# Kernel tuning notes

Hardware: AMD Instinct MI355X
Metric: run time of the kernel (lower is better)

The kernel has to match this reference:

```python
import jax, jax.numpy as jnp
import numpy as np

H, C, PQ, PV = 12, 16, 4, 8
CN = 384
INF, EPS = 1e5, 1e-7


def setup_inputs() -> dict:
    key = jax.random.key(0)
    ks = jax.random.split(key, 12)
    B, N = 2, 768
    s = jax.random.normal(ks[0], (B, N, CN), jnp.float32)
    m = jax.random.normal(ks[1], (B, N, 3, 3), jnp.float32)
    rot, _ = jnp.linalg.qr(m)  # proper orthonormal frames
    trans = jax.random.normal(ks[2], (B, N, 3), jnp.float32)
    pair_mask = jnp.ones((B, N, N), jnp.float32)
    sc = 0.02
    hc = H * C
    w_q = jax.random.normal(ks[3], (hc, CN), jnp.float32) * sc
    b_q = jnp.zeros((hc,), jnp.float32)
    w_kv = jax.random.normal(ks[4], (2 * hc, CN), jnp.float32) * sc
    b_kv = jnp.zeros((2 * hc,), jnp.float32)
    w_qp = jax.random.normal(ks[5], (H * PQ * 3, CN), jnp.float32) * sc
    b_qp = jnp.zeros((H * PQ * 3,), jnp.float32)
    w_kvp = jax.random.normal(ks[6], (H * (PQ + PV) * 3, CN), jnp.float32) * sc
    b_kvp = jnp.zeros((H * (PQ + PV) * 3,), jnp.float32)
    head_weights = jnp.full((H,), float(np.log(np.e - 1.0)), jnp.float32)  # softplus -> 1
    cod = H * (C + PV * 4)
    w_out = jax.random.normal(ks[7], (CN, cod), jnp.float32) * sc
    b_out = jnp.zeros((CN,), jnp.float32)
    return dict(s=s, rot=rot, trans=trans, pair_mask=pair_mask,
                w_q=w_q, b_q=b_q, w_kv=w_kv, b_kv=b_kv,
                w_qp=w_qp, b_qp=b_qp, w_kvp=w_kvp, b_kvp=b_kvp,
                head_weights=head_weights, w_out=w_out, b_out=b_out)


def reference(s, rot, trans, pair_mask, w_q, b_q, w_kv, b_kv, w_qp, b_qp,
              w_kvp, b_kvp, head_weights, w_out, b_out):
    B, N, _ = s.shape
    q = (s @ w_q.T + b_q).reshape(B, N, H, C)
    kv = (s @ w_kv.T + b_kv).reshape(B, N, H, 2 * C)
    k, v = kv[..., :C], kv[..., C:]

    def point_proj(wf, bf, P):
        p = s @ wf.T + bf                                   # [B,N,H*P*3]
        p = jnp.stack(jnp.split(p, 3, axis=-1), axis=-1)     # [B,N,H*P,3]
        p = jnp.einsum('bnxy,bnpy->bnpx', rot, p) + trans[:, :, None, :]
        return p.reshape(B, N, H, P, 3)

    q_pts = point_proj(w_qp, b_qp, PQ)
    kv_pts = point_proj(w_kvp, b_kvp, PQ + PV)
    k_pts, v_pts = kv_pts[..., :PQ, :], kv_pts[..., PQ:, :]

    a = jnp.einsum('bihc,bjhc->bhij', q, k) * (1.0 / (3 * C)) ** 0.5
    # [B,N,N,H,PQ] squared point distances (the big intermediate)
    d2 = jnp.sum((q_pts[:, :, None] - k_pts[:, None]) ** 2, axis=-1)
    hw = jax.nn.softplus(head_weights) * (1.0 / (3 * (PQ * 9.0 / 2))) ** 0.5
    pt_att = -0.5 * jnp.sum(d2 * hw[:, None], axis=-1)      # [B,N,N,H]
    a = a + jnp.transpose(pt_att, (0, 3, 1, 2)) + (INF * (pair_mask - 1.0))[:, None]
    a = jax.nn.softmax(a, axis=-1)                          # [B,H,N,N]

    o = jnp.einsum('bhij,bjhc->bihc', a, v).reshape(B, N, H * C)
    o_pt = jnp.einsum('bhij,bjhpc->bihpc', a, v_pts)        # [B,N,H,PV,3]
    o_pt = jnp.einsum('bnyx,bnhpy->bnhpx', rot, o_pt - trans[:, :, None, None, :])
    o_pt_norm = jnp.sqrt(jnp.sum(o_pt ** 2, axis=-1) + EPS).reshape(B, N, H * PV)
    o_pt = o_pt.reshape(B, N, H * PV, 3)
    cat = jnp.concatenate([o, o_pt[..., 0], o_pt[..., 1], o_pt[..., 2], o_pt_norm], axis=-1)
    return cat @ w_out.T + b_out
```

## Files before the change

### kernel.cpp

```cpp
#include <hip/hip_runtime.h>
#include <hip/hip_bf16.h>
#include <math.h>

typedef __attribute__((ext_vector_type(4)))  short short4v;
typedef __attribute__((ext_vector_type(8)))  short short8;
typedef __attribute__((ext_vector_type(16))) float f32x16;

#define B_   2
#define N_   768
#define CN_  384
#define H_   12
#define INF_ 100000.0f
#define EPS_ 1e-7f

#define OFF_PROJP 0
#define OFF_O     884736
#define OFF_OP    1032192
#define OFF_CAT   1253376
#define OFF_QF    1769472
#define OFF_KF    2064384
#define OFF_VT    2359296
#define OFF_SB    2949120
#define OFF_WB    3244032
#define OFF_WOB   3465216
#define OFF_MB    3575808

__device__ inline float b2f(unsigned short u) {
    union { unsigned int i; float f; } x; x.i = ((unsigned int)u) << 16; return x.f;
}
__device__ inline unsigned short f2b(float f) {
    __hip_bfloat16 h = __float2bfloat16(f);
    return *reinterpret_cast<unsigned short*>(&h);
}

__global__ __launch_bounds__(256) void prep_kernel(
    const float* __restrict__ s,
    const float* __restrict__ w_q,  const float* __restrict__ w_kv,
    const float* __restrict__ w_qp, const float* __restrict__ w_kvp,
    const float* __restrict__ w_out,
    unsigned short* __restrict__ SB, unsigned short* __restrict__ WB,
    unsigned short* __restrict__ WOBT)
{
    const long i4 = ((long)blockIdx.x * 256 + threadIdx.x) * 4;
    const float* src; unsigned short* dst; long off;
    if (i4 < 589824) {
        src = s + i4; dst = SB; off = i4;
    } else if (i4 < 1032192) {
        long e = i4 - 589824;
        int row = (int)(e / 384), c = (int)(e - (long)row * 384);
        const float* wsrc;
        if (row < 192)      wsrc = w_q   + (long)row * 384;
        else if (row < 576) wsrc = w_kv  + (long)(row - 192) * 384;
        else if (row < 720) wsrc = w_qp  + (long)(row - 576) * 384;
        else                wsrc = w_kvp + (long)(row - 720) * 384;
        src = wsrc + c; dst = WB; off = e;
    } else {
        long e = i4 - 1032192;
        int row = (int)(e / 576), c = (int)(e - (long)row * 576);
        src = w_out + e; dst = WOBT;
        off = (((long)(row >> 5) * 72 + (c >> 3)) * 32 + (row & 31)) * 8 + (c & 7);
    }
    float4 v = *(const float4*)src;
    short4v o;
    o[0] = (short)f2b(v.x); o[1] = (short)f2b(v.y);
    o[2] = (short)f2b(v.z); o[3] = (short)f2b(v.w);
    *(short4v*)(dst + off) = o;
}

__global__ __launch_bounds__(64) void proj_mb_kernel(
    const unsigned short* __restrict__ SB, const unsigned short* __restrict__ WB,
    const float* __restrict__ b_q,  const float* __restrict__ b_kv,
    const float* __restrict__ b_qp, const float* __restrict__ b_kvp,
    const float* __restrict__ mask,
    float* __restrict__ PROJP, unsigned short* __restrict__ Qf,
    unsigned short* __restrict__ Kf, unsigned short* __restrict__ Vt,
    unsigned short* __restrict__ MB)
{
    if (blockIdx.x >= 1728) {
        const int tile = blockIdx.x - 1728;
        const int jt = tile % 24;
        const int it = (tile / 24) % 24;
        const int b  = tile / 576;
        const int tt = threadIdx.x;
        const int i0 = it * 32, j0 = jt * 32;
        const float* mrow = mask + ((long)b * N_ + i0 + (tt & 31)) * N_
                          + j0 + (tt >> 5) * 4;
        union { unsigned short u[16]; short8 v[2]; } o;
        #pragma unroll
        for (int g = 0; g < 4; ++g) {
            float4 mv = *(const float4*)(mrow + 8 * g);
            o.u[g*4+0] = f2b(INF_ * (mv.x - 1.f));
            o.u[g*4+1] = f2b(INF_ * (mv.y - 1.f));
            o.u[g*4+2] = f2b(INF_ * (mv.z - 1.f));
            o.u[g*4+3] = f2b(INF_ * (mv.w - 1.f));
        }
        unsigned short* outp = MB + (long)tile * 1024 + tt * 16;
        *(short8*)(outp)     = o.v[0];
        *(short8*)(outp + 8) = o.v[1];
        return;
    }
    const int tile = blockIdx.x;
    const int tn = tile % 36, tm = tile / 36;
    const int r0 = tm * 32, c0 = tn * 32;
    const int l  = threadIdx.x;
    const int li = l & 31, hf = l >> 5;

    const unsigned short* ap = SB + (long)(r0 + li) * CN_ + hf * 8;
    const int col = c0 + li;
    const unsigned short* wb = WB + (long)col * CN_ + hf * 8;
    const float bias = (col < 192) ? b_q[col] : (col < 576) ? b_kv[col - 192]
                     : (col < 720) ? b_qp[col - 576] : b_kvp[col - 720];

    f32x16 acc = {};
    for (int k = 0; k < CN_; k += 32) {
        short8 a0 = *(const short8*)(ap + k);
        short8 a1 = *(const short8*)(ap + k + 16);
        short8 b0 = *(const short8*)(wb + k);
        short8 b1 = *(const short8*)(wb + k + 16);
        acc = __builtin_amdgcn_mfma_f32_32x32x16_bf16(a0, b0, acc, 0, 0, 0);
        acc = __builtin_amdgcn_mfma_f32_32x32x16_bf16(a1, b1, acc, 0, 0, 0);
    }
    const int row_b = r0 / N_;
    if (tn < 6) {
        const int hq = col >> 4, c = col & 15;
        const long qb = (long)(row_b * H_ + hq) * N_;
        #pragma unroll
        for (int r = 0; r < 16; ++r) {
            int row = r0 + (r & 3) + 8 * (r >> 2) + 4 * hf;
            int n = row - row_b * N_;
            Qf[(qb + n) * 32 + c] = f2b((acc[r] + bias) * 0.144337567297406f);
        }
    } else if (tn < 18) {
        const int hkv = tn - 6;
        const long kb = (long)(row_b * H_ + hkv) * N_;
        const long vb = (long)(row_b * H_ + hkv) * 24;
        #pragma unroll
        for (int r = 0; r < 16; ++r) {
            int row = r0 + (r & 3) + 8 * (r >> 2) + 4 * hf;
            int n = row - row_b * N_;
            unsigned short v = f2b(acc[r] + bias);
            if (li < 16) Kf[(kb + n) * 32 + li] = v;
            else Vt[((vb + (n >> 5)) * 64 + (li - 16)) * 32 + (n & 31)] = v;
        }
    } else {
        const int pc = col - 576;
        #pragma unroll
        for (int r = 0; r < 16; ++r) {
            int row = r0 + (r & 3) + 8 * (r >> 2) + 4 * hf;
            PROJP[(long)row * 576 + pc] = acc[r] + bias;
        }
    }
}

__global__ __launch_bounds__(128) void pack3_kernel(
    const float* __restrict__ PROJP,
    const float* __restrict__ rot, const float* __restrict__ trans,
    const float* __restrict__ head_weights,
    unsigned short* __restrict__ Qf, unsigned short* __restrict__ Kf,
    unsigned short* __restrict__ Vt)
{
    __shared__ float pp[576];
    __shared__ float rt[12];
    __shared__ float hws[12];
    __shared__ float kp2[48];
    const int bn = blockIdx.x;
    const int t  = threadIdx.x;
    const float4* src = (const float4*)(PROJP + (long)bn * 576);
    for (int d = t; d < 144; d += 128) ((float4*)pp)[d] = src[d];
    if (t < 9) rt[t]     = rot[bn * 9 + t];
    if (t < 3) rt[9 + t] = trans[bn * 3 + t];
    if (t < 12) {
        float v  = head_weights[t];
        float sp = (v > 20.f) ? v : log1pf(expf(v));
        hws[t] = sp * 0.13608276348795434f;
    }
    __syncthreads();
    const int b = bn / N_, n = bn % N_;
    for (int e = t; e < 192; e += 128) {
        if (e < 48) {
            int h = e >> 2, p = e & 3;
            float r0 = pp[     h * 4 + p];
            float r1 = pp[48 + h * 4 + p];
            float r2 = pp[96 + h * 4 + p];
            long base = ((long)(b * H_ + h) * N_ + n) * 32;
            #pragma unroll
            for (int x = 0; x < 3; ++x) {
                float o = rt[x*3]*r0 + rt[x*3+1]*r1 + rt[x*3+2]*r2 + rt[9+x];
                Qf[base + 16 + p * 3 + x] = f2b(o * hws[h]);
            }
        } else {
            int idx = e - 48;
            int h = idx / 12, pi = idx - h * 12;
            float r0 = pp[144 +       h * 12 + pi];
            float r1 = pp[144 + 144 + h * 12 + pi];
            float r2 = pp[144 + 288 + h * 12 + pi];
            float o0 = rt[0]*r0 + rt[1]*r1 + rt[2]*r2 + rt[9];
            float o1 = rt[3]*r0 + rt[4]*r1 + rt[5]*r2 + rt[10];
            float o2 = rt[6]*r0 + rt[7]*r1 + rt[8]*r2 + rt[11];
            if (pi < 4) {
                long base = ((long)(b * H_ + h) * N_ + n) * 32;
                Kf[base + 16 + pi * 3 + 0] = f2b(o0);
                Kf[base + 16 + pi * 3 + 1] = f2b(o1);
                Kf[base + 16 + pi * 3 + 2] = f2b(o2);
                kp2[h * 4 + pi] = o0*o0 + o1*o1 + o2*o2;
            } else {
                int dd = 16 + (pi - 4) * 3;
                long vb = ((long)(b * H_ + h) * 24 + (n >> 5)) * 64;
                Vt[(vb + dd + 0) * 32 + (n & 31)] = f2b(o0);
                Vt[(vb + dd + 1) * 32 + (n & 31)] = f2b(o1);
                Vt[(vb + dd + 2) * 32 + (n & 31)] = f2b(o2);
            }
        }
    }
    __syncthreads();
    if (t < 12) {
        float s2 = kp2[t*4] + kp2[t*4+1] + kp2[t*4+2] + kp2[t*4+3];
        float kc = -0.5f * hws[t] * s2;
        long base = ((long)(b * H_ + t) * N_ + n) * 32;
        unsigned short hi = f2b(kc);
        Kf[base + 28] = hi;
        Kf[base + 29] = f2b(kc - b2f(hi));
        Kf[base + 30] = 0; Kf[base + 31] = 0;
        unsigned short one = f2b(1.f);
        Qf[base + 28] = one; Qf[base + 29] = one;
        Qf[base + 30] = 0;   Qf[base + 31] = 0;
    }
}

__global__ __launch_bounds__(512) void attn2_kernel(
    const unsigned short* __restrict__ Qf, const unsigned short* __restrict__ Kf,
    const unsigned short* __restrict__ Vt, const unsigned short* __restrict__ MB,
    unsigned short* __restrict__ Og, unsigned short* __restrict__ OPg)
{
    __shared__ float red[8][64][23];
    const int blk = blockIdx.x;
    const int it = blk % 24;
    const int bh = blk / 24;
    const int hh = bh % 12;
    const int b  = bh / 12;
    const int t  = threadIdx.x;
    const int w  = t >> 6;
    const int l  = t & 63;
    const int li = l & 31;
    const int hf = l >> 5;
    const int i0 = it * 32;

    const unsigned short* qbase = Qf + ((long)bh * N_ + i0 + li) * 32 + hf * 8;
    short8 q0 = *(const short8*)(qbase);
    short8 q1 = *(const short8*)(qbase + 16);

    f32x16 acc0 = {};
    f32x16 acc1 = {};
    float m = -1e30f, lsum = 0.f;
    const unsigned short* vtb = Vt + (long)bh * 24 * 2048;
    const unsigned short* mbb = MB + ((long)(b * 24 + it)) * 24 * 1024;

    for (int jt = w * 3; jt < w * 3 + 3; ++jt) {
        const int j0 = jt * 32;
        const unsigned short* mbp = mbb + (long)jt * 1024 + l * 16;
        short8 mb0 = *(const short8*)(mbp);
        short8 mb1 = *(const short8*)(mbp + 8);
        f32x16 S;
        #pragma unroll
        for (int r = 0; r < 8; ++r) S[r]     = b2f((unsigned short)mb0[r]);
        #pragma unroll
        for (int r = 0; r < 8; ++r) S[8 + r] = b2f((unsigned short)mb1[r]);
        const unsigned short* kp = Kf + ((long)bh * N_ + j0 + li) * 32 + hf * 8;
        short8 k0 = *(const short8*)(kp);
        short8 k1 = *(const short8*)(kp + 16);
        S = __builtin_amdgcn_mfma_f32_32x32x16_bf16(k0, q0, S, 0, 0, 0);
        S = __builtin_amdgcn_mfma_f32_32x32x16_bf16(k1, q1, S, 0, 0, 0);
        float mloc = S[0];
        #pragma unroll
        for (int r = 1; r < 16; ++r) mloc = fmaxf(mloc, S[r]);
        {
            auto mm = __builtin_amdgcn_permlane32_swap(
                __float_as_int(mloc), __float_as_int(mloc), false, false);
            mloc = fmaxf(__int_as_float(mm[0]), __int_as_float(mm[1]));
        }
        float newm = fmaxf(m, mloc);
        float scale = __expf(m - newm);
        float ps = 0.f;
        f32x16 p;
        #pragma unroll
        for (int r = 0; r < 16; ++r) { p[r] = __expf(S[r] - newm); ps += p[r]; }
        {
            auto ss = __builtin_amdgcn_permlane32_swap(
                __float_as_int(ps), __float_as_int(ps), false, false);
            ps = __int_as_float(ss[0]) + __int_as_float(ss[1]);
        }
        lsum = lsum * scale + ps;
        m = newm;
        #pragma unroll
        for (int r = 0; r < 16; ++r) acc0[r] *= scale;
        #pragma unroll
        for (int r = 0; r < 4; ++r)  acc1[r] *= scale;
        int c[8];
        #pragma unroll
        for (int r = 0; r < 8; ++r) {
            asm("v_cvt_pk_bf16_f32 %0, %1, %2" : "=v"(c[r]) : "v"(p[2*r]), "v"(p[2*r+1]));
        }
        union { int w4[4]; short8 v; } bf0, bf1;
        bf0.w4[0] = c[0]; bf0.w4[1] = c[1]; bf0.w4[2] = c[2]; bf0.w4[3] = c[3];
        bf1.w4[0] = c[4]; bf1.w4[1] = c[5]; bf1.w4[2] = c[6]; bf1.w4[3] = c[7];
        const unsigned short* tb  = vtb + jt * 2048;
        const unsigned short* vr0 = tb + li * 32 + hf * 4;
        const unsigned short* vr1 = tb + (32 + li) * 32 + hf * 4;
        union { short4v h[2]; short8 v; } v00, v01, v10, v11;
        v00.h[0] = *(const short4v*)(vr0);       v00.h[1] = *(const short4v*)(vr0 + 8);
        v01.h[0] = *(const short4v*)(vr1);       v01.h[1] = *(const short4v*)(vr1 + 8);
        v10.h[0] = *(const short4v*)(vr0 + 16);  v10.h[1] = *(const short4v*)(vr0 + 24);
        v11.h[0] = *(const short4v*)(vr1 + 16);  v11.h[1] = *(const short4v*)(vr1 + 24);
        acc0 = __builtin_amdgcn_mfma_f32_32x32x16_bf16(v00.v, bf0.v, acc0, 0, 0, 0);
        acc1 = __builtin_amdgcn_mfma_f32_32x32x16_bf16(v01.v, bf0.v, acc1, 0, 0, 0);
        acc0 = __builtin_amdgcn_mfma_f32_32x32x16_bf16(v10.v, bf1.v, acc0, 0, 0, 0);
        acc1 = __builtin_amdgcn_mfma_f32_32x32x16_bf16(v11.v, bf1.v, acc1, 0, 0, 0);
    }
    float* rd = &red[w][l][0];
    rd[0] = m; rd[1] = lsum;
    #pragma unroll
    for (int r = 0; r < 16; ++r) rd[2 + r]  = acc0[r];
    #pragma unroll
    for (int r = 0; r < 4; ++r)  rd[18 + r] = acc1[r];
    __syncthreads();
    {
        const int l2 = t & 63, g = t >> 6;
        const int li2 = l2 & 31, hf2 = l2 >> 5;
        float ms = -1e30f;
        #pragma unroll
        for (int ww = 0; ww < 8; ++ww) ms = fmaxf(ms, red[ww][l2][0]);
        float wt[8]; float lf = 0.f;
        #pragma unroll
        for (int ww = 0; ww < 8; ++ww) {
            wt[ww] = __expf(red[ww][l2][0] - ms);
            lf += wt[ww] * red[ww][l2][1];
        }
        float inv = 1.f / lf;
        const int n = i0 + li2;
        #pragma unroll
        for (int rr = 0; rr < 3; ++rr) {
            int r = g + rr * 8;
            if (r < 20) {
                float v = 0.f;
                #pragma unroll
                for (int ww = 0; ww < 8; ++ww) v += wt[ww] * red[ww][l2][2 + r];
                v *= inv;
                int d = (r < 16) ? ((r & 3) + 8 * (r >> 2) + 4 * hf2)
                                 : (32 + (r - 16) + 4 * hf2);
                unsigned short ov = f2b(v);
                if (d < 16) Og [((long)(b * N_ + n)) * 192 + hh * 16 + d] = ov;
                else        OPg[((long)(b * N_ + n)) * 288 + hh * 24 + (d - 16)] = ov;
            }
        }
    }
}

__global__ __launch_bounds__(128) void cat_kernel(
    const unsigned short* __restrict__ Og, const unsigned short* __restrict__ OPg,
    const float* __restrict__ rot, const float* __restrict__ trans,
    unsigned short* __restrict__ catgT)
{
    __shared__ float cat[576];
    __shared__ float rt[12];
    const int bn = blockIdx.x;
    const int t  = threadIdx.x;
    if (t < 9) rt[t]     = rot[bn * 9 + t];
    if (t < 3) rt[9 + t] = trans[bn * 3 + t];
    for (int d = t; d < 192; d += 128) cat[d] = b2f(Og[(long)bn * 192 + d]);
    __syncthreads();
    if (t < 96) {
        float g0 = b2f(OPg[(long)bn * 288 + t * 3 + 0]) - rt[9];
        float g1 = b2f(OPg[(long)bn * 288 + t * 3 + 1]) - rt[10];
        float g2 = b2f(OPg[(long)bn * 288 + t * 3 + 2]) - rt[11];
        float l0 = rt[0]*g0 + rt[3]*g1 + rt[6]*g2;
        float l1 = rt[1]*g0 + rt[4]*g1 + rt[7]*g2;
        float l2 = rt[2]*g0 + rt[5]*g1 + rt[8]*g2;
        cat[192 + t] = l0;
        cat[288 + t] = l1;
        cat[384 + t] = l2;
        cat[480 + t] = sqrtf(l0*l0 + l1*l1 + l2*l2 + EPS_);
    }
    __syncthreads();
    const long sbase = ((long)(bn >> 5)) * 72 * 256 + (bn & 31) * 8;
    for (int d = t; d < 576; d += 128)
        catgT[sbase + (long)(d >> 3) * 256 + (d & 7)] = f2b(cat[d]);
}

__global__ __launch_bounds__(64) void out_mfma(
    const unsigned short* __restrict__ catgT,
    const unsigned short* __restrict__ WOBT,
    const float* __restrict__ b_out,
    float* __restrict__ out)
{
    const int tile = blockIdx.x;
    const int tn = tile % 12, tm = tile / 12;
    const int r0 = tm * 32, c0 = tn * 32;
    const int l  = threadIdx.x;
    const int li = l & 31, hf = l >> 5;

    const unsigned short* ab = catgT + (long)tm * 72 * 256;
    const unsigned short* wb = WOBT  + (long)tn * 72 * 256;

    f32x16 acc = {};
    for (int k = 0; k < 576; k += 32) {
        const int c = (k >> 3) + hf;
        short8 a0 = *(const short8*)(ab + (c * 32 + li) * 8);
        short8 a1 = *(const short8*)(ab + ((c + 2) * 32 + li) * 8);
        short8 b0 = *(const short8*)(wb + (c * 32 + li) * 8);
        short8 b1 = *(const short8*)(wb + ((c + 2) * 32 + li) * 8);
        acc = __builtin_amdgcn_mfma_f32_32x32x16_bf16(a0, b0, acc, 0, 0, 0);
        acc = __builtin_amdgcn_mfma_f32_32x32x16_bf16(a1, b1, acc, 0, 0, 0);
    }
    float bias = b_out[c0 + li];
    #pragma unroll
    for (int r = 0; r < 16; ++r) {
        int row = r0 + (r & 3) + 8 * (r >> 2) + 4 * hf;
        out[(long)row * 384 + c0 + li] = acc[r] + bias;
    }
}

extern "C" void kernel_launch(void* const* d_in, const int* in_sizes, int n_in,
                              void* d_out, int out_size, void* d_ws, size_t ws_size,
                              hipStream_t stream) {
    const float* s            = (const float*)d_in[0];
    const float* rot          = (const float*)d_in[1];
    const float* trans        = (const float*)d_in[2];
    const float* pair_mask    = (const float*)d_in[3];
    const float* w_q          = (const float*)d_in[4];
    const float* b_q          = (const float*)d_in[5];
    const float* w_kv         = (const float*)d_in[6];
    const float* b_kv         = (const float*)d_in[7];
    const float* w_qp         = (const float*)d_in[8];
    const float* b_qp         = (const float*)d_in[9];
    const float* w_kvp        = (const float*)d_in[10];
    const float* b_kvp        = (const float*)d_in[11];
    const float* head_weights = (const float*)d_in[12];
    const float* w_out        = (const float*)d_in[13];
    const float* b_out        = (const float*)d_in[14];
    float* out = (float*)d_out;
    float* ws  = (float*)d_ws;

    float*          PROJP = ws + OFF_PROJP;
    unsigned short* Og   = (unsigned short*)(ws + OFF_O);
    unsigned short* OPg  = (unsigned short*)(ws + OFF_OP);
    unsigned short* CATT = (unsigned short*)(ws + OFF_CAT);
    unsigned short* Qf   = (unsigned short*)(ws + OFF_QF);
    unsigned short* Kf   = (unsigned short*)(ws + OFF_KF);
    unsigned short* Vt   = (unsigned short*)(ws + OFF_VT);
    unsigned short* SB   = (unsigned short*)(ws + OFF_SB);
    unsigned short* WB   = (unsigned short*)(ws + OFF_WB);
    unsigned short* WOBT = (unsigned short*)(ws + OFF_WOB);
    unsigned short* MBp  = (unsigned short*)(ws + OFF_MB);

    prep_kernel<<<1224, 256, 0, stream>>>(s, w_q, w_kv, w_qp, w_kvp, w_out,
                                          SB, WB, WOBT);
    proj_mb_kernel<<<48 * 36 + B_ * 24 * 24, 64, 0, stream>>>(
        SB, WB, b_q, b_kv, b_qp, b_kvp, pair_mask, PROJP, Qf, Kf, Vt, MBp);
    pack3_kernel<<<B_ * N_, 128, 0, stream>>>(PROJP, rot, trans, head_weights,
                                              Qf, Kf, Vt);
    attn2_kernel<<<B_ * H_ * 24, 512, 0, stream>>>(Qf, Kf, Vt, MBp, Og, OPg);
    cat_kernel<<<B_ * N_, 128, 0, stream>>>(Og, OPg, rot, trans, CATT);
    out_mfma<<<48 * 12, 64, 0, stream>>>(CATT, WOBT, b_out, out);
}
```

Baseline: 57.69 us.

## Fuse cat/point-frame transform into output GEMM and write O directly in tiled layout

The attention kernel now writes the scalar attention output straight into the tiled bf16 layout the output GEMM reads, so the separate cat kernel is no longer needed for that part. The point-output frame transform and norm are computed inside a new fused output kernel, which stages them in shared memory and feeds them into the MFMA loop. The output GEMM now runs 4 waves per block, one per column tile, covering 3 groups. This removes one kernel launch and a global round trip. The cost is repeating the point transform in each of the 3 column-group blocks and having fewer blocks (144).

Result: faster. 56.45 us, median of 2 (-2.1%).

```diff
diff --git a/kernel.cpp b/kernel.cpp
--- a/kernel.cpp
+++ b/kernel.cpp
@@ -14,7 +14,6 @@
 #define EPS_ 1e-7f
 
 #define OFF_PROJP 0
-#define OFF_O     884736
 #define OFF_OP    1032192
 #define OFF_CAT   1253376
 #define OFF_QF    1769472
@@ -230,7 +229,7 @@
 __global__ __launch_bounds__(512) void attn2_kernel(
     const unsigned short* __restrict__ Qf, const unsigned short* __restrict__ Kf,
     const unsigned short* __restrict__ Vt, const unsigned short* __restrict__ MB,
-    unsigned short* __restrict__ Og, unsigned short* __restrict__ OPg)
+    unsigned short* __restrict__ CATT, unsigned short* __restrict__ OPg)
 {
     __shared__ float red[8][64][23];
     const int blk = blockIdx.x;
@@ -337,6 +336,7 @@
         }
         float inv = 1.f / lf;
         const int n = i0 + li2;
+        const long ctile = ((long)(b * 24 + it)) * 72 * 256 + li2 * 8;
         #pragma unroll
         for (int rr = 0; rr < 3; ++rr) {
             int r = g + rr * 8;
@@ -348,61 +348,64 @@
                 int d = (r < 16) ? ((r & 3) + 8 * (r >> 2) + 4 * hf2)
                                  : (32 + (r - 16) + 4 * hf2);
                 unsigned short ov = f2b(v);
-                if (d < 16) Og [((long)(b * N_ + n)) * 192 + hh * 16 + d] = ov;
-                else        OPg[((long)(b * N_ + n)) * 288 + hh * 24 + (d - 16)] = ov;
+                if (d < 16) {
+                    int c = hh * 16 + d;
+                    CATT[ctile + (long)(c >> 3) * 256 + (c & 7)] = ov;
+                } else {
+                    OPg[((long)(b * N_ + n)) * 288 + hh * 24 + (d - 16)] = ov;
+                }
             }
         }
     }
 }
 
-__global__ __launch_bounds__(128) void cat_kernel(
-    const unsigned short* __restrict__ Og, const unsigned short* __restrict__ OPg,
+__global__ __launch_bounds__(256) void out_fused2(
+    const unsigned short* __restrict__ CATT, const unsigned short* __restrict__ OPg,
     const float* __restrict__ rot, const float* __restrict__ trans,
-    unsigned short* __restrict__ catgT)
-{
-    __shared__ float cat[576];
-    __shared__ float rt[12];
-    const int bn = blockIdx.x;
-    const int t  = threadIdx.x;
-    if (t < 9) rt[t]     = rot[bn * 9 + t];
-    if (t < 3) rt[9 + t] = trans[bn * 3 + t];
-    for (int d = t; d < 192; d += 128) cat[d] = b2f(Og[(long)bn * 192 + d]);
-    __syncthreads();
-    if (t < 96) {
-        float g0 = b2f(OPg[(long)bn * 288 + t * 3 + 0]) - rt[9];
-        float g1 = b2f(OPg[(long)bn * 288 + t * 3 + 1]) - rt[10];
-        float g2 = b2f(OPg[(long)bn * 288 + t * 3 + 2]) - rt[11];
-        float l0 = rt[0]*g0 + rt[3]*g1 + rt[6]*g2;
-        float l1 = rt[1]*g0 + rt[4]*g1 + rt[7]*g2;
-        float l2 = rt[2]*g0 + rt[5]*g1 + rt[8]*g2;
-        cat[192 + t] = l0;
-        cat[288 + t] = l1;
-        cat[384 + t] = l2;
-        cat[480 + t] = sqrtf(l0*l0 + l1*l1 + l2*l2 + EPS_);
-    }
-    __syncthreads();
-    const long sbase = ((long)(bn >> 5)) * 72 * 256 + (bn & 31) * 8;
-    for (int d = t; d < 576; d += 128)
-        catgT[sbase + (long)(d >> 3) * 256 + (d & 7)] = f2b(cat[d]);
-}
-
-__global__ __launch_bounds__(64) void out_mfma(
-    const unsigned short* __restrict__ catgT,
-    const unsigned short* __restrict__ WOBT,
-    const float* __restrict__ b_out,
+    const unsigned short* __restrict__ WOBT, const float* __restrict__ b_out,
     float* __restrict__ out)
 {
-    const int tile = blockIdx.x;
-    const int tn = tile % 12, tm = tile / 12;
-    const int r0 = tm * 32, c0 = tn * 32;
-    const int l  = threadIdx.x;
+    __shared__ unsigned short op_s[32][288];
+    __shared__ unsigned short catp[48][32][8];
+    __shared__ float rt_s[32][12];
+    const int blk = blockIdx.x;
+    const int tm = blk / 3, tng = blk % 3;
+    const int r0 = tm * 32;
+    const int t  = threadIdx.x;
+
+    for (int e = t; e < 32 * 36; e += 256) {
+        int rr = e / 36, c8 = e - rr * 36;
+        *(short8*)&op_s[rr][c8 * 8] = *(const short8*)(OPg + (long)(r0 + rr) * 288 + c8 * 8);
+    }
+    for (int e = t; e < 32 * 12; e += 256) {
+        int rr = e / 12, c = e - rr * 12;
+        rt_s[rr][c] = (c < 9) ? rot[(long)(r0 + rr) * 9 + c]
+                              : trans[(long)(r0 + rr) * 3 + (c - 9)];
+    }
+    __syncthreads();
+    for (int e = t; e < 3072; e += 256) {
+        int rr = e / 96, pt = e - (e / 96) * 96;
+        const float* rp = rt_s[rr];
+        float g0 = b2f(op_s[rr][pt * 3 + 0]) - rp[9];
+        float g1 = b2f(op_s[rr][pt * 3 + 1]) - rp[10];
+        float g2 = b2f(op_s[rr][pt * 3 + 2]) - rp[11];
+        float l0 = rp[0]*g0 + rp[3]*g1 + rp[6]*g2;
+        float l1 = rp[1]*g0 + rp[4]*g1 + rp[7]*g2;
+        float l2 = rp[2]*g0 + rp[5]*g1 + rp[8]*g2;
+        int c;
+        c = 192 + pt; catp[(c >> 3) - 24][rr][c & 7] = f2b(l0);
+        c = 288 + pt; catp[(c >> 3) - 24][rr][c & 7] = f2b(l1);
+        c = 384 + pt; catp[(c >> 3) - 24][rr][c & 7] = f2b(l2);
+        c = 480 + pt; catp[(c >> 3) - 24][rr][c & 7] = f2b(sqrtf(l0*l0 + l1*l1 + l2*l2 + EPS_));
+    }
+    __syncthreads();
+    const int wv = t >> 6, l = t & 63;
     const int li = l & 31, hf = l >> 5;
-
-    const unsigned short* ab = catgT + (long)tm * 72 * 256;
-    const unsigned short* wb = WOBT  + (long)tn * 72 * 256;
-
+    const int tn = tng * 4 + wv;
+    const unsigned short* ab = CATT + (long)tm * 72 * 256;
+    const unsigned short* wb = WOBT + (long)tn * 72 * 256;
     f32x16 acc = {};
-    for (int k = 0; k < 576; k += 32) {
+    for (int k = 0; k < 192; k += 32) {
         const int c = (k >> 3) + hf;
         short8 a0 = *(const short8*)(ab + (c * 32 + li) * 8);
         short8 a1 = *(const short8*)(ab + ((c + 2) * 32 + li) * 8);
@@ -411,11 +414,21 @@
         acc = __builtin_amdgcn_mfma_f32_32x32x16_bf16(a0, b0, acc, 0, 0, 0);
         acc = __builtin_amdgcn_mfma_f32_32x32x16_bf16(a1, b1, acc, 0, 0, 0);
     }
-    float bias = b_out[c0 + li];
+    for (int k = 192; k < 576; k += 32) {
+        const int cg = (k >> 3) + hf;
+        const int cl = cg - 24;
+        short8 a0 = *(const short8*)&catp[cl][li][0];
+        short8 a1 = *(const short8*)&catp[cl + 2][li][0];
+        short8 b0 = *(const short8*)(wb + (cg * 32 + li) * 8);
+        short8 b1 = *(const short8*)(wb + ((cg + 2) * 32 + li) * 8);
+        acc = __builtin_amdgcn_mfma_f32_32x32x16_bf16(a0, b0, acc, 0, 0, 0);
+        acc = __builtin_amdgcn_mfma_f32_32x32x16_bf16(a1, b1, acc, 0, 0, 0);
+    }
+    float bias = b_out[tn * 32 + li];
     #pragma unroll
     for (int r = 0; r < 16; ++r) {
         int row = r0 + (r & 3) + 8 * (r >> 2) + 4 * hf;
-        out[(long)row * 384 + c0 + li] = acc[r] + bias;
+        out[(long)row * 384 + tn * 32 + li] = acc[r] + bias;
     }
 }
 
@@ -441,7 +454,6 @@
     float* ws  = (float*)d_ws;
 
     float*          PROJP = ws + OFF_PROJP;
-    unsigned short* Og   = (unsigned short*)(ws + OFF_O);
     unsigned short* OPg  = (unsigned short*)(ws + OFF_OP);
     unsigned short* CATT = (unsigned short*)(ws + OFF_CAT);
     unsigned short* Qf   = (unsigned short*)(ws + OFF_QF);
@@ -458,7 +470,6 @@
         SB, WB, b_q, b_kv, b_qp, b_kvp, pair_mask, PROJP, Qf, Kf, Vt, MBp);
     pack3_kernel<<<B_ * N_, 128, 0, stream>>>(PROJP, rot, trans, head_weights,
                                               Qf, Kf, Vt);
-    attn2_kernel<<<B_ * H_ * 24, 512, 0, stream>>>(Qf, Kf, Vt, MBp, Og, OPg);
-    cat_kernel<<<B_ * N_, 128, 0, stream>>>(Og, OPg, rot, trans, CATT);
-    out_mfma<<<48 * 12, 64, 0, stream>>>(CATT, WOBT, b_out, out);
-}
+    attn2_kernel<<<B_ * H_ * 24, 512, 0, stream>>>(Qf, Kf, Vt, MBp, CATT, OPg);
+    out_fused2<<<48 * 3, 256, 0, stream>>>(CATT, OPg, rot, trans, WOBT, b_out, out);
+}
```
